# Optimization experiments

Measured on AMD Instinct MI355X. Metric: run time of the kernel, lower is better.

The kernel has to match this reference:

```python
import jax, jax.numpy as jnp
import numpy as np

B, C, G = 8, 64, 65536
IN_DIM, OUT_DIM = 64, 64
SLOPE = 0.1


def setup_inputs() -> dict:
    key = jax.random.key(0)
    ks = jax.random.split(key, 5)
    features = jax.random.normal(ks[0], (B, C, G), dtype=jnp.float32)
    # Conv2d(in*2, out, 1, bias=False) weights, squeezed to [out, in*2]
    W0 = jax.random.normal(ks[1], (OUT_DIM, IN_DIM * 2), dtype=jnp.float32) * (1.0 / np.sqrt(IN_DIM * 2))
    W1 = jax.random.normal(ks[2], (OUT_DIM, OUT_DIM * 2), dtype=jnp.float32) * (1.0 / np.sqrt(OUT_DIM * 2))
    W2 = jax.random.normal(ks[3], (OUT_DIM, OUT_DIM * 2), dtype=jnp.float32) * (1.0 / np.sqrt(OUT_DIM * 2))
    W3 = jax.random.normal(ks[4], (OUT_DIM, OUT_DIM * 2), dtype=jnp.float32) * (1.0 / np.sqrt(OUT_DIM * 2))
    return {"features": features, "W0": W0, "W1": W1, "W2": W2, "W3": W3}


def _layer(x, W):
    # x: [B, C, G]; tile the first group's features and build (x, x - x0)
    x0 = x[:, :, :1]                               # [B, C, 1]
    h = jnp.concatenate([x, x - x0], axis=1)       # [B, 2C, G]
    # 1x1 conv == pointwise linear over channels
    y = jnp.einsum("oc,bcg->bog", W, h)            # [B, O, G]
    return jax.nn.leaky_relu(y, negative_slope=SLOPE)


def reference(features, W0, W1, W2, W3):
    x = features
    for W in (W0, W1, W2, W3):
        x = _layer(x, W)
    return jnp.max(x, axis=-1)                     # [B, O]
```

## Files before the change

kernel.cpp:

```cpp
#include <hip/hip_runtime.h>


#define G_TOT 65536

typedef _Float16 hf2 __attribute__((ext_vector_type(2)));
typedef _Float16 hf4 __attribute__((ext_vector_type(4)));
typedef _Float16 hf8 __attribute__((ext_vector_type(8)));
typedef float float4_ __attribute__((ext_vector_type(4)));

static __device__ __forceinline__ hf2 pkh(float x, float y) {
    return __builtin_bit_cast(hf2, __builtin_amdgcn_cvt_pkrtz(x, y));
}


__global__ __launch_bounds__(256) void ge_prep(
    const float* __restrict__ feat,
    const float* __restrict__ W0, const float* __restrict__ W1,
    const float* __restrict__ W2, const float* __restrict__ W3,
    float* __restrict__ ws)
{
    const int tid = threadIdx.x;
    const int blk = blockIdx.x;
    __shared__ float lw[64][129];
    __shared__ float x0[2][64];

    if (blk == 8) {
        unsigned* maxenc = (unsigned*)(ws + 18432);
        maxenc[tid] = 0u; maxenc[tid + 256] = 0u;
        for (int i = tid; i < 4 * 64 * 64; i += 256) {
            int l = i >> 12, o = (i >> 6) & 63, c = i & 63;
            const float* Wl = (l == 0) ? W0 : (l == 1) ? W1 : (l == 2) ? W2 : W3;
            ws[i] = Wl[o * 128 + c] + Wl[o * 128 + 64 + c];
        }
        return;
    }

    const int b = blk;
    if (tid < 64) x0[0][tid] = feat[(size_t)(b * 64 + tid) * G_TOT];
    float* nbias = ws + 16384;
    for (int l = 0; l < 4; ++l) {
        const float* Wl = (l == 0) ? W0 : (l == 1) ? W1 : (l == 2) ? W2 : W3;
        for (int i = tid; i < 64 * 128; i += 256) lw[i >> 7][i & 127] = Wl[i];
        __syncthreads();
        if (tid < 64) {
            const int o = tid;
            const float* src = x0[l & 1];
            float s1 = 0.f, s2 = 0.f;
            for (int c = 0; c < 64; ++c) {
                float xv = src[c];
                s1 += lw[o][c] * xv;
                s2 += lw[o][64 + c] * xv;
            }
            nbias[b * 256 + l * 64 + o] = -s2;
            x0[(l & 1) ^ 1][o] = fmaxf(s1, 0.1f * s1);
        }
        __syncthreads();
    }
}

__global__ __launch_bounds__(256, 2) void ge_main(
    const float* __restrict__ feat,
    const float* __restrict__ ws_wa,
    const float* __restrict__ nbias,
    unsigned* __restrict__ maxenc)
{
    __shared__ _Float16 lws[16384];
    __shared__ float lbias[256];
    __shared__ float blockmax[4][64];
    const int tid = threadIdx.x;
    const int b = blockIdx.x >> 7;

    for (int gi = tid; gi < 4096; gi += 256) {
        int hi = gi & 1, ln = (gi >> 1) & 63, f = gi >> 7;
        int pr = f & 1, mt = (f >> 1) & 3, l = f >> 3;
        int o = (mt << 4) + (ln & 15);
        int c = (((pr << 1) + hi) << 4) + ((ln >> 4) << 2);
        float4_ wv = *(const float4_*)&ws_wa[((l << 6) + o) * 64 + c];
        union { hf2 h2[2]; hf4 h4; } u;
        u.h2[0] = pkh(wv[0], wv[1]);
        u.h2[1] = pkh(wv[2], wv[3]);
        *(hf4*)&lws[gi << 2] = u.h4;
    }
    lbias[tid] = nbias[(b << 8) + tid];
    __syncthreads();

    const int w = tid >> 6, lane = tid & 63, q = lane >> 4, n = lane & 15;
    const int g0 = ((blockIdx.x & 127) << 9) + (w << 7);
    const float* Xrow = feat + (size_t)b * 64 * G_TOT + (size_t)(q << 2) * G_TOT;
    const hf4 k01 = { (_Float16)0.1f, (_Float16)0.1f, (_Float16)0.1f, (_Float16)0.1f };

    float rmax[4][4];
#pragma unroll
    for (int mt = 0; mt < 4; ++mt)
#pragma unroll
        for (int j = 0; j < 4; ++j) rmax[mt][j] = -__builtin_inff();

    float cur[16];
    {
        int gcol = g0 + n;
#pragma unroll
        for (int kf = 0; kf < 4; ++kf)
#pragma unroll
            for (int r = 0; r < 4; ++r)
                cur[kf * 4 + r] = Xrow[(size_t)((kf << 4) + r) * G_TOT + gcol];
    }

#pragma unroll 1
    for (int nt = 0; nt < 8; ++nt) {
        float nxt[16];
        if (nt < 7) {
            int gcol = g0 + ((nt + 1) << 4) + n;
#pragma unroll
            for (int kf = 0; kf < 4; ++kf)
#pragma unroll
                for (int r = 0; r < 4; ++r)
                    nxt[kf * 4 + r] = Xrow[(size_t)((kf << 4) + r) * G_TOT + gcol];
        }

        hf4 bf[4];
#pragma unroll
        for (int kf = 0; kf < 4; ++kf) {
            union { hf2 h2[2]; hf4 h4; } u;
            u.h2[0] = pkh(cur[kf * 4 + 0], cur[kf * 4 + 1]);
            u.h2[1] = pkh(cur[kf * 4 + 2], cur[kf * 4 + 3]);
            bf[kf] = u.h4;
        }

#pragma unroll
        for (int l = 0; l < 4; ++l) {
            float4_ acc[4];
#pragma unroll
            for (int mt = 0; mt < 4; ++mt)
                acc[mt] = *(const float4_*)&lbias[(l << 6) + (mt << 4) + (q << 2)];
#pragma unroll
            for (int mt = 0; mt < 4; ++mt) {
#pragma unroll
                for (int pr = 0; pr < 2; ++pr) {
                    union { hf8 h8; hf4 h4[2]; } ua;
                    ua.h8 = *(const hf8*)&lws[((((((l << 2) + mt) << 1) + pr) << 6) + lane) << 3];
                    acc[mt] = __builtin_amdgcn_mfma_f32_16x16x16f16(ua.h4[0], bf[(pr << 1) + 0], acc[mt], 0, 0, 0);
                    acc[mt] = __builtin_amdgcn_mfma_f32_16x16x16f16(ua.h4[1], bf[(pr << 1) + 1], acc[mt], 0, 0, 0);
                }
            }
            if (l < 3) {
#pragma unroll
                for (int mt = 0; mt < 4; ++mt) {
                    union { hf2 h2[2]; hf4 h4; } u;
                    u.h2[0] = pkh(acc[mt][0], acc[mt][1]);
                    u.h2[1] = pkh(acc[mt][2], acc[mt][3]);
                    hf4 h = u.h4;
                    h = __builtin_elementwise_max(h, h * k01);
                    bf[mt] = h;
                }
            } else {
#pragma unroll
                for (int mt = 0; mt < 4; ++mt)
#pragma unroll
                    for (int j = 0; j < 4; ++j)
                        rmax[mt][j] = fmaxf(rmax[mt][j], acc[mt][j]);
            }
        }
        if (nt < 7) {
#pragma unroll
            for (int i = 0; i < 16; ++i) cur[i] = nxt[i];
        }
    }

#pragma unroll
    for (int mt = 0; mt < 4; ++mt)
#pragma unroll
        for (int j = 0; j < 4; ++j) {
            float v = rmax[mt][j];
            v = fmaxf(v, __shfl_xor(v, 1, 64));
            v = fmaxf(v, __shfl_xor(v, 2, 64));
            v = fmaxf(v, __shfl_xor(v, 4, 64));
            v = fmaxf(v, __shfl_xor(v, 8, 64));
            rmax[mt][j] = fmaxf(v, 0.1f * v);
        }
    if (n == 0) {
#pragma unroll
        for (int mt = 0; mt < 4; ++mt)
#pragma unroll
            for (int j = 0; j < 4; ++j)
                blockmax[w][(mt << 4) + (q << 2) + j] = rmax[mt][j];
    }
    __syncthreads();
    if (tid < 64) {
        float v = fmaxf(fmaxf(blockmax[0][tid], blockmax[1][tid]),
                        fmaxf(blockmax[2][tid], blockmax[3][tid]));
        unsigned s = __float_as_uint(v);
        unsigned enc = (s & 0x80000000u) ? ~s : (s | 0x80000000u);
        atomicMax(&maxenc[b * 64 + tid], enc);
    }
}

__global__ void ge_final(const unsigned* __restrict__ maxenc, float* __restrict__ out)
{
    int i = threadIdx.x;
    if (i < 512) {
        unsigned u = maxenc[i];
        unsigned s = (u & 0x80000000u) ? (u ^ 0x80000000u) : ~u;
        out[i] = __uint_as_float(s);
    }
}

extern "C" void kernel_launch(void* const* d_in, const int* in_sizes, int n_in,
                              void* d_out, int out_size, void* d_ws, size_t ws_size,
                              hipStream_t stream) {
    const float* feat = (const float*)d_in[0];
    const float* W0 = (const float*)d_in[1];
    const float* W1 = (const float*)d_in[2];
    const float* W2 = (const float*)d_in[3];
    const float* W3 = (const float*)d_in[4];
    float* ws = (float*)d_ws;
    unsigned* maxenc = (unsigned*)(ws + 18432);

    ge_prep<<<9, 256, 0, stream>>>(feat, W0, W1, W2, W3, ws);
    ge_main<<<1024, 256, 0, stream>>>(feat, ws, ws + 16384, maxenc);
    ge_final<<<1, 512, 0, stream>>>(maxenc, (float*)d_out);
}
```

Before: 220.0 us.

## Pre-pack fp16 MFMA weights in prep, hold them in registers, halve grid

The prep kernel now writes the combined weights as fp16, already laid out in the MFMA fragment order. The main kernel loads all of them into registers (32 hf8 per lane) instead of staging and converting them through shared memory in every block. The grid is halved so each wave handles 256 columns over 16 iterations, which amortises the setup. The last layer's bias and leaky-ReLU are moved after the max into the final kernel, which is exact because both are monotonic. The cost is much higher register pressure, which may cut occupancy or cause spills, and fewer blocks to cover the GPU.

```diff
diff --git a/kernel.cpp b/kernel.cpp
--- a/kernel.cpp
+++ b/kernel.cpp
@@ -27,10 +27,16 @@
     if (blk == 8) {
         unsigned* maxenc = (unsigned*)(ws + 18432);
         maxenc[tid] = 0u; maxenc[tid + 256] = 0u;
-        for (int i = tid; i < 4 * 64 * 64; i += 256) {
-            int l = i >> 12, o = (i >> 6) & 63, c = i & 63;
+        _Float16* wf = (_Float16*)ws;
+        for (int ci = tid; ci < 8192; ci += 256) {
+            int f = ci >> 8, ln = (ci >> 2) & 63, h2 = ci & 3;
+            int l = f >> 3, mt = (f >> 1) & 3, pr = f & 1;
+            int o = (mt << 4) + (ln & 15);
+            int c = (pr << 5) + ((h2 >> 1) << 4) + ((ln >> 4) << 2) + ((h2 & 1) << 1);
             const float* Wl = (l == 0) ? W0 : (l == 1) ? W1 : (l == 2) ? W2 : W3;
-            ws[i] = Wl[o * 128 + c] + Wl[o * 128 + 64 + c];
+            float a0 = Wl[o * 128 + c]     + Wl[o * 128 + 64 + c];
+            float a1 = Wl[o * 128 + c + 1] + Wl[o * 128 + 64 + c + 1];
+            *(hf2*)&wf[ci << 1] = pkh(a0, a1);
         }
         return;
     }
@@ -60,34 +66,32 @@
 
 __global__ __launch_bounds__(256, 2) void ge_main(
     const float* __restrict__ feat,
-    const float* __restrict__ ws_wa,
+    const float* __restrict__ ws_wf,
     const float* __restrict__ nbias,
     unsigned* __restrict__ maxenc)
 {
-    __shared__ _Float16 lws[16384];
     __shared__ float lbias[256];
     __shared__ float blockmax[4][64];
     const int tid = threadIdx.x;
-    const int b = blockIdx.x >> 7;
-
-    for (int gi = tid; gi < 4096; gi += 256) {
-        int hi = gi & 1, ln = (gi >> 1) & 63, f = gi >> 7;
-        int pr = f & 1, mt = (f >> 1) & 3, l = f >> 3;
-        int o = (mt << 4) + (ln & 15);
-        int c = (((pr << 1) + hi) << 4) + ((ln >> 4) << 2);
-        float4_ wv = *(const float4_*)&ws_wa[((l << 6) + o) * 64 + c];
-        union { hf2 h2[2]; hf4 h4; } u;
-        u.h2[0] = pkh(wv[0], wv[1]);
-        u.h2[1] = pkh(wv[2], wv[3]);
-        *(hf4*)&lws[gi << 2] = u.h4;
-    }
+    const int b = blockIdx.x >> 6;
+    const int w = tid >> 6, lane = tid & 63, q = lane >> 4, n = lane & 15;
+
     lbias[tid] = nbias[(b << 8) + tid];
-    __syncthreads();
-
-    const int w = tid >> 6, lane = tid & 63, q = lane >> 4, n = lane & 15;
-    const int g0 = ((blockIdx.x & 127) << 9) + (w << 7);
+
+    hf8 wfr[4][4][2];
+    {
+        const hf8* wp = (const hf8*)ws_wf;
+#pragma unroll
+        for (int l = 0; l < 4; ++l)
+#pragma unroll
+            for (int mt = 0; mt < 4; ++mt)
+#pragma unroll
+                for (int pr = 0; pr < 2; ++pr)
+                    wfr[l][mt][pr] = wp[((((((l << 2) + mt) << 1) + pr)) << 6) + lane];
+    }
+
+    const int g0 = ((blockIdx.x & 63) << 10) + (w << 8);
     const float* Xrow = feat + (size_t)b * 64 * G_TOT + (size_t)(q << 2) * G_TOT;
-    const hf4 k01 = { (_Float16)0.1f, (_Float16)0.1f, (_Float16)0.1f, (_Float16)0.1f };
 
     float rmax[4][4];
 #pragma unroll
@@ -95,20 +99,28 @@
 #pragma unroll
         for (int j = 0; j < 4; ++j) rmax[mt][j] = -__builtin_inff();
 
-    float cur[16];
+    float nxt[16];
     {
         int gcol = g0 + n;
 #pragma unroll
         for (int kf = 0; kf < 4; ++kf)
 #pragma unroll
             for (int r = 0; r < 4; ++r)
-                cur[kf * 4 + r] = Xrow[(size_t)((kf << 4) + r) * G_TOT + gcol];
-    }
+                nxt[kf * 4 + r] = Xrow[(size_t)((kf << 4) + r) * G_TOT + gcol];
+    }
+    __syncthreads();
 
 #pragma unroll 1
-    for (int nt = 0; nt < 8; ++nt) {
-        float nxt[16];
-        if (nt < 7) {
+    for (int nt = 0; nt < 16; ++nt) {
+        hf4 bf[4];
+#pragma unroll
+        for (int kf = 0; kf < 4; ++kf) {
+            union { hf2 h2[2]; hf4 h4; } u;
+            u.h2[0] = pkh(nxt[kf * 4 + 0], nxt[kf * 4 + 1]);
+            u.h2[1] = pkh(nxt[kf * 4 + 2], nxt[kf * 4 + 3]);
+            bf[kf] = u.h4;
+        }
+        if (nt < 15) {
             int gcol = g0 + ((nt + 1) << 4) + n;
 #pragma unroll
             for (int kf = 0; kf < 4; ++kf)
@@ -117,27 +129,23 @@
                     nxt[kf * 4 + r] = Xrow[(size_t)((kf << 4) + r) * G_TOT + gcol];
         }
 
-        hf4 bf[4];
-#pragma unroll
-        for (int kf = 0; kf < 4; ++kf) {
-            union { hf2 h2[2]; hf4 h4; } u;
-            u.h2[0] = pkh(cur[kf * 4 + 0], cur[kf * 4 + 1]);
-            u.h2[1] = pkh(cur[kf * 4 + 2], cur[kf * 4 + 3]);
-            bf[kf] = u.h4;
-        }
-
 #pragma unroll
         for (int l = 0; l < 4; ++l) {
             float4_ acc[4];
 #pragma unroll
-            for (int mt = 0; mt < 4; ++mt)
-                acc[mt] = *(const float4_*)&lbias[(l << 6) + (mt << 4) + (q << 2)];
+            for (int mt = 0; mt < 4; ++mt) {
+                if (l < 3) {
+                    acc[mt] = *(const float4_*)&lbias[(l << 6) + (mt << 4) + (q << 2)];
+                } else {
+                    acc[mt] = float4_{0.f, 0.f, 0.f, 0.f};
+                }
+            }
 #pragma unroll
             for (int mt = 0; mt < 4; ++mt) {
 #pragma unroll
                 for (int pr = 0; pr < 2; ++pr) {
                     union { hf8 h8; hf4 h4[2]; } ua;
-                    ua.h8 = *(const hf8*)&lws[((((((l << 2) + mt) << 1) + pr) << 6) + lane) << 3];
+                    ua.h8 = wfr[l][mt][pr];
                     acc[mt] = __builtin_amdgcn_mfma_f32_16x16x16f16(ua.h4[0], bf[(pr << 1) + 0], acc[mt], 0, 0, 0);
                     acc[mt] = __builtin_amdgcn_mfma_f32_16x16x16f16(ua.h4[1], bf[(pr << 1) + 1], acc[mt], 0, 0, 0);
                 }
@@ -149,7 +157,7 @@
                     u.h2[0] = pkh(acc[mt][0], acc[mt][1]);
                     u.h2[1] = pkh(acc[mt][2], acc[mt][3]);
                     hf4 h = u.h4;
-                    h = __builtin_elementwise_max(h, h * k01);
+                    h = __builtin_elementwise_max(h, h * hf4{(_Float16)0.1f, (_Float16)0.1f, (_Float16)0.1f, (_Float16)0.1f});
                     bf[mt] = h;
                 }
             } else {
@@ -159,10 +167,6 @@
                     for (int j = 0; j < 4; ++j)
                         rmax[mt][j] = fmaxf(rmax[mt][j], acc[mt][j]);
             }
-        }
-        if (nt < 7) {
-#pragma unroll
-            for (int i = 0; i < 16; ++i) cur[i] = nxt[i];
         }
     }
 
@@ -175,7 +179,7 @@
             v = fmaxf(v, __shfl_xor(v, 2, 64));
             v = fmaxf(v, __shfl_xor(v, 4, 64));
             v = fmaxf(v, __shfl_xor(v, 8, 64));
-            rmax[mt][j] = fmaxf(v, 0.1f * v);
+            rmax[mt][j] = v;
         }
     if (n == 0) {
 #pragma unroll
@@ -194,13 +198,16 @@
     }
 }
 
-__global__ void ge_final(const unsigned* __restrict__ maxenc, float* __restrict__ out)
+__global__ void ge_final(const unsigned* __restrict__ maxenc,
+                         const float* __restrict__ nbias,
+                         float* __restrict__ out)
 {
     int i = threadIdx.x;
     if (i < 512) {
         unsigned u = maxenc[i];
         unsigned s = (u & 0x80000000u) ? (u ^ 0x80000000u) : ~u;
-        out[i] = __uint_as_float(s);
+        float v = __uint_as_float(s) + nbias[((i >> 6) << 8) + 192 + (i & 63)];
+        out[i] = fmaxf(v, 0.1f * v);
     }
 }
 
@@ -216,6 +223,6 @@
     unsigned* maxenc = (unsigned*)(ws + 18432);
 
     ge_prep<<<9, 256, 0, stream>>>(feat, W0, W1, W2, W3, ws);
-    ge_main<<<1024, 256, 0, stream>>>(feat, ws, ws + 16384, maxenc);
-    ge_final<<<1, 512, 0, stream>>>(maxenc, (float*)d_out);
-}
+    ge_main<<<512, 256, 0, stream>>>(feat, ws, ws + 16384, maxenc);
+    ge_final<<<1, 512, 0, stream>>>(maxenc, ws + 16384, (float*)d_out);
+}
```

Result: no change. 217.4 us (-1.2%).
